# Performance work log

Measured on AMD Instinct MI355X. Metric: run time of the kernel, lower is better.

The kernel has to match this reference:

```python
import jax, jax.numpy as jnp
import numpy as np

MAXDISP = 4  # matches init_kwargs


def setup_inputs() -> dict:
    key = jax.random.key(0)
    k1, k2 = jax.random.split(key)
    shape = (4, 64, 64, 128)  # (b, c, H, W)
    return {
        "refimg_fea": jax.random.normal(k1, shape, dtype=jnp.float32),
        "targetimg_fea": jax.random.normal(k2, shape, dtype=jnp.float32),
    }


def _correlation(ref, tgt, md=MAXDISP):
    # cost[b,c,i,j,y,x] = ref[b,c,y,x] * tgt[b,c,y+(j-md), x+(i-md)] when in
    # bounds, else 0 (the torch code pre-fills with zeros). Zero-padding the
    # target reproduces the out-of-bounds zeros exactly, since the product with
    # a padded zero is 0 and leaky_relu(0) == 0.
    b, c, H, W = ref.shape
    D = 2 * md + 1
    tpad = jnp.pad(tgt, ((0, 0), (0, 0), (md, md), (md, md)))

    def shift(i, j):
        # i indexes the width offset (ind), j the height offset (indd),
        # matching cost[:, :, i, j] in the original double loop.
        return jax.lax.dynamic_slice(tpad, (0, 0, j, i), (b, c, H, W))

    idx = jnp.arange(D)
    # shifts: [D_i, D_j, b, c, H, W]
    shifts = jax.vmap(lambda i: jax.vmap(lambda j: shift(i, j))(idx))(idx)
    cost = jax.nn.leaky_relu(ref[None, None] * shifts, negative_slope=0.1)
    # -> (b, c, D_i, D_j, H, W)
    return jnp.transpose(cost, (2, 3, 0, 1, 4, 5))


def reference(refimg_fea, targetimg_fea):
    return _correlation(refimg_fea, targetimg_fea, MAXDISP)
```

## Files before the change

### kernel.cpp

```cpp
#include <hip/hip_runtime.h>

#define MD 4
#define DD 9
#define B  4
#define C  64
#define H  64
#define W  128
#define HW (H * W)

#define LROW  136
#define LROWS 72
#define LDS_F (LROWS * LROW)

typedef float f32x4 __attribute__((ext_vector_type(4)));

__device__ __forceinline__ f32x4 lrelu4(f32x4 p) {
    f32x4 o;
    o.x = fmaxf(p.x, 0.1f * p.x);
    o.y = fmaxf(p.y, 0.1f * p.y);
    o.z = fmaxf(p.z, 0.1f * p.z);
    o.w = fmaxf(p.w, 0.1f * p.w);
    return o;
}

__global__ __launch_bounds__(256) void corr_kernel(const float* __restrict__ ref,
                                                   const float* __restrict__ tgt,
                                                   float* __restrict__ out) {
    __shared__ __align__(16) float ldsT[LDS_F];

    const unsigned t  = threadIdx.x;
    const unsigned bc = blockIdx.x / 3u;
    const unsigned i0 = (blockIdx.x % 3u) * 3u;
    const unsigned x4 = t & 31u;
    const unsigned x  = x4 * 4u;
    const unsigned yw = t >> 5;

    const float* refp = ref + (size_t)bc * HW;
    const float* tgtp = tgt + (size_t)bc * HW;

    f32x4 r8[8];
    #pragma unroll
    for (int s = 0; s < 8; ++s)
        r8[s] = *reinterpret_cast<const f32x4*>(refp + (size_t)(s * 8 + yw) * W + x);

    for (unsigned k = 0; k < 3; ++k) {
        const unsigned i  = i0 + k;
        const unsigned sh = 8u - i;

        __syncthreads();

        #pragma unroll
        for (int z = 0; z < 10; ++z) {
            unsigned idx = (unsigned)z * 256u + t;
            if (idx < LDS_F / 4)
                reinterpret_cast<f32x4*>(ldsT)[idx] = (f32x4){0.f, 0.f, 0.f, 0.f};
        }
        __syncthreads();

        #pragma unroll
        for (int z = 0; z < 8; ++z) {
            unsigned idx = (unsigned)z * 256u + t;
            unsigned row = idx >> 5;
            unsigned c4  = idx & 31u;
            f32x4 g = *reinterpret_cast<const f32x4*>(tgtp + (size_t)idx * 4u);
            unsigned base = (row + MD) * LROW + c4 * 4u + sh;
            ldsT[base + 0] = g.x;
            ldsT[base + 1] = g.y;
            ldsT[base + 2] = g.z;
            ldsT[base + 3] = g.w;
        }
        __syncthreads();

        float* outu = out + ((size_t)bc * (DD * DD) + (size_t)i * DD) * HW;
        #pragma unroll
        for (int j = 0; j < DD; ++j) {
            float* oj = outu + (size_t)j * HW;
            #pragma unroll
            for (int s = 0; s < 8; ++s) {
                const unsigned y = (unsigned)s * 8u + yw;
                const f32x4 w = *reinterpret_cast<const f32x4*>(
                    &ldsT[(y + (unsigned)j) * LROW + x + 4u]);
                __builtin_nontemporal_store(
                    lrelu4(r8[s] * w),
                    reinterpret_cast<f32x4*>(oj + (size_t)y * W + x));
            }
        }
    }
}

extern "C" void kernel_launch(void* const* d_in, const int* in_sizes, int n_in,
                              void* d_out, int out_size, void* d_ws, size_t ws_size,
                              hipStream_t stream) {
    const float* ref = (const float*)d_in[0];
    const float* tgt = (const float*)d_in[1];
    float* out = (float*)d_out;

    corr_kernel<<<768, 256, 0, stream>>>(ref, tgt, out);
}
```

Before: 148.1 us.

## Drop LDS staging; read shifted target rows directly via templated width offset

Removes the shared-memory staging of the padded target tile, including its zero-fill and barriers. Each thread now loads the needed target vectors straight from global memory, using neighbor float4 loads and a compile-time width shift per template instantiation. Parallelism also changes from 768 blocks handling three width offsets each to 2304 blocks handling one offset each, so there are more blocks but each block re-reads ref and tgt from L2. The kernel is store-bound on output writes, so the gain mainly comes from removing synchronization and LDS traffic, at the cost of more global and cache loads.

```diff
diff --git a/kernel.cpp b/kernel.cpp
--- a/kernel.cpp
+++ b/kernel.cpp
@@ -8,83 +8,84 @@
 #define W  128
 #define HW (H * W)
 
-#define LROW  136
-#define LROWS 72
-#define LDS_F (LROWS * LROW)
-
 typedef float f32x4 __attribute__((ext_vector_type(4)));
 
-__device__ __forceinline__ f32x4 lrelu4(f32x4 p) {
-    f32x4 o;
-    o.x = fmaxf(p.x, 0.1f * p.x);
-    o.y = fmaxf(p.y, 0.1f * p.y);
-    o.z = fmaxf(p.z, 0.1f * p.z);
-    o.w = fmaxf(p.w, 0.1f * p.w);
-    return o;
+
+template<int I>
+__device__ __forceinline__ void run_i(const float* __restrict__ refp,
+                                      const float* __restrict__ tgtp,
+                                      float* __restrict__ outp,
+                                      unsigned t) {
+    constexpr int d = I - MD;
+    const unsigned x4 = t & 31u;
+    const unsigned yw = t >> 5;
+    const unsigned x  = x4 * 4u;
+
+    f32x4 r8[8];
+    #pragma unroll
+    for (int s = 0; s < 8; ++s)
+        r8[s] = *reinterpret_cast<const f32x4*>(refp + (unsigned)(s * 8 + yw) * W + x);
+
+    #pragma unroll
+    for (int j = 0; j < DD; ++j) {
+        float* oj = outp + (size_t)j * HW;
+        #pragma unroll
+        for (int s = 0; s < 8; ++s) {
+            const int y  = s * 8 + (int)yw;
+            const int ty = y + j - MD;
+            const bool vrow = (ty >= 0) & (ty < H);
+            const int tyc = ty < 0 ? 0 : (ty > H - 1 ? H - 1 : ty);
+            const float* trow = tgtp + (unsigned)tyc * W;
+
+            f32x4 m = {0.f, 0.f, 0.f, 0.f};
+            f32x4 c;
+            f32x4 p = {0.f, 0.f, 0.f, 0.f};
+            if constexpr (d < 0) {
+                if (x4 > 0) m = *reinterpret_cast<const f32x4*>(trow + x - 4);
+            }
+            c = *reinterpret_cast<const f32x4*>(trow + x);
+            if constexpr (d > 0) {
+                if (x4 < 31u) p = *reinterpret_cast<const f32x4*>(trow + x + 4);
+            }
+            const float tw[12] = {m.x, m.y, m.z, m.w,
+                                  c.x, c.y, c.z, c.w,
+                                  p.x, p.y, p.z, p.w};
+            f32x4 o;
+            #pragma unroll
+            for (int e = 0; e < 4; ++e) {
+                const float wv = tw[4 + d + e];
+                float pv = r8[s][e] * wv;
+                pv = fmaxf(pv, 0.1f * pv);
+                o[e] = vrow ? pv : 0.0f;
+            }
+            __builtin_nontemporal_store(
+                o, reinterpret_cast<f32x4*>(oj + (unsigned)y * W + x));
+        }
+    }
 }
 
 __global__ __launch_bounds__(256) void corr_kernel(const float* __restrict__ ref,
                                                    const float* __restrict__ tgt,
                                                    float* __restrict__ out) {
-    __shared__ __align__(16) float ldsT[LDS_F];
-
-    const unsigned t  = threadIdx.x;
-    const unsigned bc = blockIdx.x / 3u;
-    const unsigned i0 = (blockIdx.x % 3u) * 3u;
-    const unsigned x4 = t & 31u;
-    const unsigned x  = x4 * 4u;
-    const unsigned yw = t >> 5;
+    const unsigned blk = blockIdx.x;
+    const unsigned bc  = blk / 9u;
+    const unsigned i   = blk - bc * 9u;
 
     const float* refp = ref + (size_t)bc * HW;
     const float* tgtp = tgt + (size_t)bc * HW;
+    float* outp = out + ((size_t)bc * (DD * DD) + (size_t)i * DD) * HW;
+    const unsigned t = threadIdx.x;
 
-    f32x4 r8[8];
-    #pragma unroll
-    for (int s = 0; s < 8; ++s)
-        r8[s] = *reinterpret_cast<const f32x4*>(refp + (size_t)(s * 8 + yw) * W + x);
-
-    for (unsigned k = 0; k < 3; ++k) {
-        const unsigned i  = i0 + k;
-        const unsigned sh = 8u - i;
-
-        __syncthreads();
-
-        #pragma unroll
-        for (int z = 0; z < 10; ++z) {
-            unsigned idx = (unsigned)z * 256u + t;
-            if (idx < LDS_F / 4)
-                reinterpret_cast<f32x4*>(ldsT)[idx] = (f32x4){0.f, 0.f, 0.f, 0.f};
-        }
-        __syncthreads();
-
-        #pragma unroll
-        for (int z = 0; z < 8; ++z) {
-            unsigned idx = (unsigned)z * 256u + t;
-            unsigned row = idx >> 5;
-            unsigned c4  = idx & 31u;
-            f32x4 g = *reinterpret_cast<const f32x4*>(tgtp + (size_t)idx * 4u);
-            unsigned base = (row + MD) * LROW + c4 * 4u + sh;
-            ldsT[base + 0] = g.x;
-            ldsT[base + 1] = g.y;
-            ldsT[base + 2] = g.z;
-            ldsT[base + 3] = g.w;
-        }
-        __syncthreads();
-
-        float* outu = out + ((size_t)bc * (DD * DD) + (size_t)i * DD) * HW;
-        #pragma unroll
-        for (int j = 0; j < DD; ++j) {
-            float* oj = outu + (size_t)j * HW;
-            #pragma unroll
-            for (int s = 0; s < 8; ++s) {
-                const unsigned y = (unsigned)s * 8u + yw;
-                const f32x4 w = *reinterpret_cast<const f32x4*>(
-                    &ldsT[(y + (unsigned)j) * LROW + x + 4u]);
-                __builtin_nontemporal_store(
-                    lrelu4(r8[s] * w),
-                    reinterpret_cast<f32x4*>(oj + (size_t)y * W + x));
-            }
-        }
+    switch (i) {
+        case 0: run_i<0>(refp, tgtp, outp, t); break;
+        case 1: run_i<1>(refp, tgtp, outp, t); break;
+        case 2: run_i<2>(refp, tgtp, outp, t); break;
+        case 3: run_i<3>(refp, tgtp, outp, t); break;
+        case 4: run_i<4>(refp, tgtp, outp, t); break;
+        case 5: run_i<5>(refp, tgtp, outp, t); break;
+        case 6: run_i<6>(refp, tgtp, outp, t); break;
+        case 7: run_i<7>(refp, tgtp, outp, t); break;
+        default: run_i<8>(refp, tgtp, outp, t); break;
     }
 }
 
@@ -95,5 +96,5 @@
     const float* tgt = (const float*)d_in[1];
     float* out = (float*)d_out;
 
-    corr_kernel<<<768, 256, 0, stream>>>(ref, tgt, out);
+    corr_kernel<<<B * C * DD, 256, 0, stream>>>(ref, tgt, out);
 }
```

New measurement: 151.1 us. +2.0%, slower.

## Give each block a single width offset and shift in registers

Applied to the files above, without the earlier changes.

Each block now handles one width offset instead of three, giving 2304 blocks instead of 768. The shared-memory tile is loaded once with aligned vector stores, and only the padding halo is zeroed rather than the whole buffer. The horizontal shift is applied by reading two aligned vectors and selecting lanes at compile time, using a template per offset dispatched through a switch. It also drops the nontemporal hint on output stores. The costs are that the target and ref are reloaded once per offset (9x instead of 3x) and that code size grows.

```diff
diff --git a/kernel.cpp b/kernel.cpp
--- a/kernel.cpp
+++ b/kernel.cpp
@@ -10,7 +10,7 @@
 
 #define LROW  136
 #define LROWS 72
-#define LDS_F (LROWS * LROW)
+#define LDSW  (LROWS * LROW)
 
 typedef float f32x4 __attribute__((ext_vector_type(4)));
 
@@ -23,68 +23,92 @@
     return o;
 }
 
+template<int I>
+__device__ __forceinline__ void compute_i(const float* __restrict__ ldsT,
+                                          const f32x4* r8,
+                                          float* __restrict__ outu,
+                                          unsigned x4, unsigned yw) {
+    constexpr int d = I - MD;
+    const unsigned x = x4 * 4u;
+
+    #pragma unroll
+    for (int j = 0; j < DD; ++j) {
+        float* oj = outu + (size_t)j * HW;
+        #pragma unroll
+        for (int s = 0; s < 8; ++s) {
+            const unsigned y    = (unsigned)s * 8u + yw;
+            const unsigned rowb = (y + (unsigned)j) * LROW;
+            f32x4 t;
+            if constexpr (d == 0) {
+                t = *reinterpret_cast<const f32x4*>(ldsT + rowb + 4u + x);
+            } else if constexpr (d < 0) {
+                const f32x4 m = *reinterpret_cast<const f32x4*>(ldsT + rowb + x);
+                const f32x4 c = *reinterpret_cast<const f32x4*>(ldsT + rowb + 4u + x);
+                const float tw[8] = {m.x, m.y, m.z, m.w, c.x, c.y, c.z, c.w};
+                t = (f32x4){tw[4 + d], tw[5 + d], tw[6 + d], tw[7 + d]};
+            } else {
+                const f32x4 c = *reinterpret_cast<const f32x4*>(ldsT + rowb + 4u + x);
+                const f32x4 p = *reinterpret_cast<const f32x4*>(ldsT + rowb + 8u + x);
+                const float tw[8] = {c.x, c.y, c.z, c.w, p.x, p.y, p.z, p.w};
+                t = (f32x4){tw[d], tw[d + 1], tw[d + 2], tw[d + 3]};
+            }
+            *reinterpret_cast<f32x4*>(oj + (size_t)y * W + x) = lrelu4(r8[s] * t);
+        }
+    }
+}
+
 __global__ __launch_bounds__(256) void corr_kernel(const float* __restrict__ ref,
                                                    const float* __restrict__ tgt,
                                                    float* __restrict__ out) {
-    __shared__ __align__(16) float ldsT[LDS_F];
+    __shared__ __align__(16) float ldsT[LDSW];
 
     const unsigned t  = threadIdx.x;
-    const unsigned bc = blockIdx.x / 3u;
-    const unsigned i0 = (blockIdx.x % 3u) * 3u;
+    const unsigned bc = blockIdx.x / 9u;
+    const unsigned i  = blockIdx.x - bc * 9u;
     const unsigned x4 = t & 31u;
+    const unsigned yw = t >> 5;
     const unsigned x  = x4 * 4u;
-    const unsigned yw = t >> 5;
 
     const float* refp = ref + (size_t)bc * HW;
     const float* tgtp = tgt + (size_t)bc * HW;
+
+    const f32x4 z4 = {0.f, 0.f, 0.f, 0.f};
+    if (t < 136u) {
+        reinterpret_cast<f32x4*>(ldsT)[t] = z4;
+        reinterpret_cast<f32x4*>(ldsT + 68 * LROW)[t] = z4;
+    } else if (t < 200u) {
+        const unsigned r = 4u + (t - 136u);
+        *reinterpret_cast<f32x4*>(ldsT + r * LROW) = z4;
+        *reinterpret_cast<f32x4*>(ldsT + r * LROW + 132u) = z4;
+    }
+
+    #pragma unroll
+    for (int z = 0; z < 8; ++z) {
+        const unsigned idx = (unsigned)z * 256u + t;
+        const unsigned row = idx >> 5;
+        const unsigned c4  = idx & 31u;
+        const f32x4 g = *reinterpret_cast<const f32x4*>(tgtp + (size_t)idx * 4u);
+        *reinterpret_cast<f32x4*>(ldsT + (row + 4u) * LROW + 4u + c4 * 4u) = g;
+    }
 
     f32x4 r8[8];
     #pragma unroll
     for (int s = 0; s < 8; ++s)
         r8[s] = *reinterpret_cast<const f32x4*>(refp + (size_t)(s * 8 + yw) * W + x);
 
-    for (unsigned k = 0; k < 3; ++k) {
-        const unsigned i  = i0 + k;
-        const unsigned sh = 8u - i;
+    __syncthreads();
 
-        __syncthreads();
-
-        #pragma unroll
-        for (int z = 0; z < 10; ++z) {
-            unsigned idx = (unsigned)z * 256u + t;
-            if (idx < LDS_F / 4)
-                reinterpret_cast<f32x4*>(ldsT)[idx] = (f32x4){0.f, 0.f, 0.f, 0.f};
-        }
-        __syncthreads();
-
-        #pragma unroll
-        for (int z = 0; z < 8; ++z) {
-            unsigned idx = (unsigned)z * 256u + t;
-            unsigned row = idx >> 5;
-            unsigned c4  = idx & 31u;
-            f32x4 g = *reinterpret_cast<const f32x4*>(tgtp + (size_t)idx * 4u);
-            unsigned base = (row + MD) * LROW + c4 * 4u + sh;
-            ldsT[base + 0] = g.x;
-            ldsT[base + 1] = g.y;
-            ldsT[base + 2] = g.z;
-            ldsT[base + 3] = g.w;
-        }
-        __syncthreads();
-
-        float* outu = out + ((size_t)bc * (DD * DD) + (size_t)i * DD) * HW;
-        #pragma unroll
-        for (int j = 0; j < DD; ++j) {
-            float* oj = outu + (size_t)j * HW;
-            #pragma unroll
-            for (int s = 0; s < 8; ++s) {
-                const unsigned y = (unsigned)s * 8u + yw;
-                const f32x4 w = *reinterpret_cast<const f32x4*>(
-                    &ldsT[(y + (unsigned)j) * LROW + x + 4u]);
-                __builtin_nontemporal_store(
-                    lrelu4(r8[s] * w),
-                    reinterpret_cast<f32x4*>(oj + (size_t)y * W + x));
-            }
-        }
+    float* outu = out + ((size_t)bc * (DD * DD) + (size_t)i * DD) * HW;
+    switch (i) {
+        case 0: compute_i<0>(ldsT, r8, outu, x4, yw); break;
+        case 1: compute_i<1>(ldsT, r8, outu, x4, yw); break;
+        case 2: compute_i<2>(ldsT, r8, outu, x4, yw); break;
+        case 3: compute_i<3>(ldsT, r8, outu, x4, yw); break;
+        case 4: compute_i<4>(ldsT, r8, outu, x4, yw); break;
+        case 5: compute_i<5>(ldsT, r8, outu, x4, yw); break;
+        case 6: compute_i<6>(ldsT, r8, outu, x4, yw); break;
+        case 7: compute_i<7>(ldsT, r8, outu, x4, yw); break;
+        default: compute_i<8>(ldsT, r8, outu, x4, yw); break;
     }
 }
 
@@ -95,5 +119,5 @@
     const float* tgt = (const float*)d_in[1];
     float* out = (float*)d_out;
 
-    corr_kernel<<<768, 256, 0, stream>>>(ref, tgt, out);
+    corr_kernel<<<B * C * DD, 256, 0, stream>>>(ref, tgt, out);
 }
```

New measurement: 138.1 us. -6.7%, faster.
